# Kernel tuning notes

Measured on AMD Instinct MI355X. Metric: run time of the kernel, lower is better.

## Reference

```python
import jax, jax.numpy as jnp
import numpy as np

N_NODES = 100000
N_EDGES = 1600000
IN_DIM, HID_DIM, OUT_DIM = 128, 256, 512
BN_EPS = 1e-5


def setup_inputs() -> dict:
    key = jax.random.key(0)
    ks = jax.random.split(key, 10)
    x = jax.random.normal(ks[0], (N_NODES, IN_DIM), dtype=jnp.float32)
    edge_index = jax.random.randint(ks[1], (2, N_EDGES), 0, N_NODES, dtype=jnp.int64)
    def lin(k, o, i):
        return jax.random.normal(k, (o, i), dtype=jnp.float32) * (1.0 / np.sqrt(i))
    return {
        "x": x,
        "edge_index": edge_index,
        # SAGEConv 1: in_dim -> hidden_dim (lin_l has bias, lin_r has none)
        "W1l": lin(ks[2], HID_DIM, IN_DIM),
        "b1": jnp.zeros((HID_DIM,), dtype=jnp.float32),
        "W1r": lin(ks[3], HID_DIM, IN_DIM),
        # BatchNorm1d(hidden_dim)
        "gamma": jnp.ones((HID_DIM,), dtype=jnp.float32),
        "beta": jnp.zeros((HID_DIM,), dtype=jnp.float32),
        # SAGEConv 2: hidden_dim -> gnn_out_dim
        "W2l": lin(ks[4], OUT_DIM, HID_DIM),
        "b2": jnp.zeros((OUT_DIM,), dtype=jnp.float32),
        "W2r": lin(ks[5], OUT_DIM, HID_DIM),
    }


def _sage_max(h, src, dst, Wl, b, Wr, n_nodes):
    # gather source features, max-aggregate onto destination nodes
    agg = jax.ops.segment_max(h[src], dst, num_segments=n_nodes)  # [N, D]
    agg = jnp.where(jnp.isneginf(agg), 0.0, agg)  # PyG fills empty segments with 0
    return agg @ Wl.T + b + h @ Wr.T


def reference(x, edge_index, W1l, b1, W1r, gamma, beta, W2l, b2, W2r):
    src, dst = edge_index[0], edge_index[1]
    n = x.shape[0]
    # layer 1: SAGEConv(in_dim, hidden_dim, aggr='max')
    h = _sage_max(x, src, dst, W1l, b1, W1r, n)
    # BatchNorm1d (batch statistics), Dropout is identity in eval; no activation in 'sage' branch
    mean = jnp.mean(h, axis=0)
    var = jnp.var(h, axis=0)
    h = gamma * (h - mean) * jax.lax.rsqrt(var + BN_EPS) + beta
    # layer 2: SAGEConv(hidden_dim, gnn_out_dim, aggr='max')
    out = _sage_max(h, src, dst, W2l, b2, W2r, n)
    return out
```

## Files before the change

kernel.cpp:

```cpp
#include <hip/hip_runtime.h>
#include <hip/hip_bf16.h>
#include <stdint.h>

#define N_NODES 100000
#define N_EDGES 1600000
#define IN_DIM 128
#define HID_DIM 256
#define OUT_DIM 512
#define NBUK 391
#define BCAP 8192
#define EPB 4096

typedef __attribute__((ext_vector_type(4))) float f32x4;
typedef __attribute__((ext_vector_type(8))) short bf16x8;

__device__ __forceinline__ float bf16lo(uint32_t u){ uint32_t b = u << 16; return __builtin_bit_cast(float, b); }
__device__ __forceinline__ float bf16hi(uint32_t u){ uint32_t b = u & 0xffff0000u; return __builtin_bit_cast(float, b); }
__device__ __forceinline__ uint16_t f32_to_bf16(float f){
  uint32_t u = __builtin_bit_cast(uint32_t, f);
  uint32_t r = (u + 0x7fffu + ((u >> 16) & 1u)) >> 16;
  return (uint16_t)r;
}
__device__ __forceinline__ uint32_t pack_bf16_exact(float lo, float hi){
  return (__builtin_bit_cast(uint32_t, hi) & 0xffff0000u) | (__builtin_bit_cast(uint32_t, lo) >> 16);
}
__device__ __forceinline__ uint32_t pack_bf16_rne(float lo, float hi){
  return (uint32_t)f32_to_bf16(lo) | ((uint32_t)f32_to_bf16(hi) << 16);
}
__device__ __forceinline__ void gl2lds16(const void* g, void* l){
  __builtin_amdgcn_global_load_lds(
      (const __attribute__((address_space(1))) uint32_t*)g,
      (__attribute__((address_space(3))) uint32_t*)l, 16, 0, 0);
}

__global__ void k_convx(const float* __restrict__ x, uint16_t* __restrict__ X1x,
                        int* __restrict__ gcur, float* __restrict__ sum,
                        float* __restrict__ sumsq){
  if (blockIdx.x == 12500){
    const int t = threadIdx.x;
    for (int i = t; i < NBUK; i += 256) gcur[i] = i << 13;
    sum[t] = 0.f; sumsq[t] = 0.f;
    return;
  }
  const int idx = blockIdx.x * 256 + threadIdx.x;
  const int n = idx >> 5, q = idx & 31;
  const float4 v = *(const float4*)(x + (long)n * 128 + q * 4);
  ushort4 o;
  o.x = f32_to_bf16(v.x); o.y = f32_to_bf16(v.y);
  o.z = f32_to_bf16(v.z); o.w = f32_to_bf16(v.w);
  *(ushort4*)(X1x + (long)n * 128 + q * 4) = o;
}

__global__ void k_bucket(const int* __restrict__ src, const int* __restrict__ dst,
                         int* __restrict__ gcur, int* __restrict__ ebuk){
  __shared__ int hist[NBUK], curs[NBUK], base[NBUK];
  const int tid = threadIdx.x;
  const int e0 = blockIdx.x * EPB;
  for (int t = tid; t < NBUK; t += 256) hist[t] = 0;
  __syncthreads();
  for (int i = 0; i < EPB; i += 256){
    int e = e0 + i + tid;
    if (e < N_EDGES) atomicAdd(&hist[dst[e] >> 8], 1);
  }
  __syncthreads();
  for (int t = tid; t < NBUK; t += 256){
    int h = hist[t];
    base[t] = h ? atomicAdd(&gcur[t], h) : 0;
    curs[t] = 0;
  }
  __syncthreads();
  for (int i = 0; i < EPB; i += 256){
    int e = e0 + i + tid;
    if (e < N_EDGES){
      int d = dst[e];
      int b = d >> 8;
      int idx = atomicAdd(&curs[b], 1);
      int pos = base[b] + idx;
      if (pos < ((b + 1) << 13))
        ebuk[pos] = ((d & 255) << 17) | src[e];
    }
  }
}

__global__ __launch_bounds__(256)
void k_fillc(const int* __restrict__ gcur, const int* __restrict__ ebuk,
             int* __restrict__ row_start, int* __restrict__ esrc){
  __shared__ int ebuf[BCAP];
  __shared__ int cnt[256];
  __shared__ int wtot[4];
  __shared__ int red[4];
  const int b = blockIdx.x, tid = threadIdx.x, lane = tid & 63, wv = tid >> 6;
  const int nodebase = b << 8;
  const int nodecnt = min(256, N_NODES - nodebase);
  int accb = 0;
  for (int t = tid; t < b; t += 256) accb += gcur[t] - (t << 13);
  #pragma unroll
  for (int d = 32; d > 0; d >>= 1) accb += __shfl_xor(accb, d);
  if (lane == 0) red[wv] = accb;
  int size_b = gcur[b] - (b << 13);
  if (size_b > BCAP) size_b = BCAP;
  cnt[tid] = 0;
  for (int i = tid; i < size_b; i += 256) ebuf[i] = ebuk[(b << 13) + i];
  __syncthreads();
  const int bs = red[0] + red[1] + red[2] + red[3];
  for (int i = tid; i < size_b; i += 256) atomicAdd(&cnt[ebuf[i] >> 17], 1);
  __syncthreads();
  const int c = cnt[tid];
  int v = c;
  #pragma unroll
  for (int d = 1; d < 64; d <<= 1){ int t = __shfl_up(v, d); if (lane >= d) v += t; }
  if (lane == 63) wtot[wv] = v;
  __syncthreads();
  if (tid < 4){
    int t = wtot[tid];
    #pragma unroll
    for (int d = 1; d < 4; d <<= 1){ int u = __shfl_up(t, d); if (tid >= d) t += u; }
    wtot[tid] = t;
  }
  __syncthreads();
  const int excl = (wv ? wtot[wv - 1] : 0) + (v - c);
  if (tid < nodecnt) row_start[nodebase + tid] = bs + excl;
  if (b == NBUK - 1 && tid == 0) row_start[N_NODES] = N_EDGES;
  cnt[tid] = excl;
  __syncthreads();
  for (int i = tid; i < size_b; i += 256){
    int p = ebuf[i];
    int pos = atomicAdd(&cnt[p >> 17], 1);
    esrc[bs + pos] = p & 0x1FFFF;
  }
}

__global__ void k_w1(const float* __restrict__ W1l, const float* __restrict__ W1r,
                     uint16_t* __restrict__ W1cat){
  int idx = blockIdx.x * 256 + threadIdx.x;
  int j = idx >> 8, k = idx & 255;
  float v = (k < 128) ? W1l[j * 128 + k] : W1r[j * 128 + (k - 128)];
  W1cat[idx] = f32_to_bf16(v);
}

__global__ void k_w2(const float* __restrict__ W2l, const float* __restrict__ W2r,
                     const float* __restrict__ b2, const float* __restrict__ sum,
                     const float* __restrict__ sumsq, const float* __restrict__ gamma,
                     const float* __restrict__ beta, uint16_t* __restrict__ W2cat,
                     float* __restrict__ bias2, float* __restrict__ scale_g,
                     float* __restrict__ shift_g){
  __shared__ float sc_s[256], sh_s[256];
  const int tid = threadIdx.x;
  {
    const float inv_n = 1.0f / (float)N_NODES;
    float mean = sum[tid] * inv_n;
    float var = sumsq[tid] * inv_n - mean * mean;
    float sc = gamma[tid] * rsqrtf(var + 1e-5f);
    float sh = beta[tid] - mean * sc;
    sc_s[tid] = sc; sh_s[tid] = sh;
    if (blockIdx.x == 0){ scale_g[tid] = sc; shift_g[tid] = sh; }
  }
  __syncthreads();
  const int wid = (blockIdx.x * 256 + tid) >> 6;
  const int lane = tid & 63;
  float part = 0.f;
  #pragma unroll
  for (int t = 0; t < 4; t++){
    int k = t * 64 + lane;
    float wl = W2l[(long)wid * 256 + k];
    W2cat[(long)wid * 512 + k] = f32_to_bf16(wl);
    float wr = W2r[(long)wid * 256 + k];
    W2cat[(long)wid * 512 + 256 + k] = f32_to_bf16(wr * sc_s[k]);
    part += sh_s[k] * wr;
  }
  #pragma unroll
  for (int d = 32; d > 0; d >>= 1) part += __shfl_xor(part, d);
  if (lane == 0) bias2[wid] = b2[wid] + part;
}

__global__ void k_agg1(const uint32_t* __restrict__ X1x, const int* __restrict__ row_start,
                       const int* __restrict__ esrc, uint32_t* __restrict__ X1agg){
  const int wid = (blockIdx.x * 256 + threadIdx.x) >> 6;
  const int lane = threadIdx.x & 63;
  if (wid >= N_NODES) return;
  const int grp = lane >> 4, li = lane & 15;
  const int s0 = row_start[wid], s1 = row_start[wid + 1];
  float m[8];
  #pragma unroll
  for (int j = 0; j < 8; j++) m[j] = -INFINITY;

  #define ACC1(u)                                        \
    m[0] = fmaxf(m[0], bf16lo(u.x)); m[1] = fmaxf(m[1], bf16hi(u.x)); \
    m[2] = fmaxf(m[2], bf16lo(u.y)); m[3] = fmaxf(m[3], bf16hi(u.y)); \
    m[4] = fmaxf(m[4], bf16lo(u.z)); m[5] = fmaxf(m[5], bf16hi(u.z)); \
    m[6] = fmaxf(m[6], bf16lo(u.w)); m[7] = fmaxf(m[7], bf16hi(u.w));

  int e = s0 + grp;
  for (; e + 12 < s1; e += 16){
    const uint4 ua = *(const uint4*)(X1x + (long)esrc[e] * 64 + li * 4);
    const uint4 ub = *(const uint4*)(X1x + (long)esrc[e + 4] * 64 + li * 4);
    const uint4 uc = *(const uint4*)(X1x + (long)esrc[e + 8] * 64 + li * 4);
    const uint4 ud = *(const uint4*)(X1x + (long)esrc[e + 12] * 64 + li * 4);
    ACC1(ua); ACC1(ub); ACC1(uc); ACC1(ud);
  }
  for (; e < s1; e += 4){
    const uint4 u = *(const uint4*)(X1x + (long)esrc[e] * 64 + li * 4);
    ACC1(u);
  }
  #undef ACC1
  #pragma unroll
  for (int j = 0; j < 8; j++){
    m[j] = fmaxf(m[j], __shfl_xor(m[j], 16));
    m[j] = fmaxf(m[j], __shfl_xor(m[j], 32));
  }
  if (grp == 0){
    uint4 o;
    if (s1 == s0){ o.x = o.y = o.z = o.w = 0u; }
    else {
      o.x = pack_bf16_exact(m[0], m[1]);
      o.y = pack_bf16_exact(m[2], m[3]);
      o.z = pack_bf16_exact(m[4], m[5]);
      o.w = pack_bf16_exact(m[6], m[7]);
    }
    *(uint4*)(X1agg + (long)wid * 64 + li * 4) = o;
  }
}

__global__ void k_agg2(const uint32_t* __restrict__ X2h, const int* __restrict__ row_start,
                       const int* __restrict__ esrc, const float* __restrict__ scale,
                       const float* __restrict__ shift, uint32_t* __restrict__ X2agg){
  const int wid = (blockIdx.x * 256 + threadIdx.x) >> 6;
  const int lane = threadIdx.x & 63;
  if (wid >= N_NODES) return;
  const int half = lane >> 5, li = lane & 31;
  const int c0 = li * 8;
  const float4 sca = *(const float4*)(scale + c0);
  const float4 scb = *(const float4*)(scale + c0 + 4);
  const float4 sha = *(const float4*)(shift + c0);
  const float4 shb = *(const float4*)(shift + c0 + 4);
  const int s0 = row_start[wid], s1 = row_start[wid + 1];
  float m[8];
  #pragma unroll
  for (int j = 0; j < 8; j++) m[j] = -INFINITY;

  #define ACC8(u)                                                   \
    m[0] = fmaxf(m[0], fmaf(bf16lo(u.x), sca.x, sha.x));            \
    m[1] = fmaxf(m[1], fmaf(bf16hi(u.x), sca.y, sha.y));            \
    m[2] = fmaxf(m[2], fmaf(bf16lo(u.y), sca.z, sha.z));            \
    m[3] = fmaxf(m[3], fmaf(bf16hi(u.y), sca.w, sha.w));            \
    m[4] = fmaxf(m[4], fmaf(bf16lo(u.z), scb.x, shb.x));            \
    m[5] = fmaxf(m[5], fmaf(bf16hi(u.z), scb.y, shb.y));            \
    m[6] = fmaxf(m[6], fmaf(bf16lo(u.w), scb.z, shb.z));            \
    m[7] = fmaxf(m[7], fmaf(bf16hi(u.w), scb.w, shb.w));

  int e = s0 + half;
  for (; e + 6 < s1; e += 8){
    const uint4 ua = *(const uint4*)(X2h + (long)esrc[e] * 128 + li * 4);
    const uint4 ub = *(const uint4*)(X2h + (long)esrc[e + 2] * 128 + li * 4);
    const uint4 uc = *(const uint4*)(X2h + (long)esrc[e + 4] * 128 + li * 4);
    const uint4 ud = *(const uint4*)(X2h + (long)esrc[e + 6] * 128 + li * 4);
    ACC8(ua); ACC8(ub); ACC8(uc); ACC8(ud);
  }
  for (; e < s1; e += 2){
    const uint4 u = *(const uint4*)(X2h + (long)esrc[e] * 128 + li * 4);
    ACC8(u);
  }
  #undef ACC8
  #pragma unroll
  for (int j = 0; j < 8; j++) m[j] = fmaxf(m[j], __shfl_xor(m[j], 32));
  if (half == 0){
    uint4 o;
    if (s1 == s0){ o.x = 0u; o.y = 0u; o.z = 0u; o.w = 0u; }
    else {
      o.x = pack_bf16_rne(m[0], m[1]);
      o.y = pack_bf16_rne(m[2], m[3]);
      o.z = pack_bf16_rne(m[4], m[5]);
      o.w = pack_bf16_rne(m[6], m[7]);
    }
    *(uint4*)(X2agg + (long)wid * 128 + li * 4) = o;
  }
}

template<int KT, bool EPI1>
__global__ __launch_bounds__(256, 2)
void k_gemm(const uint16_t* __restrict__ Alo, const uint16_t* __restrict__ Ahi,
            const uint16_t* __restrict__ B, const float* __restrict__ bias,
            uint16_t* __restrict__ outb, float* __restrict__ outf,
            float* __restrict__ sum, float* __restrict__ sumsq)
{
  constexpr int NSTEPS = KT / 64;
  constexpr int HSTEPS = NSTEPS / 2;
  constexpr int NT = EPI1 ? 256 : 512;
  __shared__ uint8_t lds[2][32768];
  const int tid = threadIdx.x, lane = tid & 63, wv = tid >> 6;
  const int wvm = wv >> 1, wvn = wv & 1;
  const int nblk = blockIdx.x, mblk = blockIdx.y;

  f32x4 acc[4][4] = {};

  const int srow = wv * 32 + (lane >> 3);
  const int skb  = (lane & 7) * 16;

  const uint8_t* asrc_lo[4];
  const uint8_t* asrc_hi[4];
  const uint8_t* bsrc[4];
  #pragma unroll
  for (int i = 0; i < 4; i++){
    int row = srow + i * 8;
    int kbsw = skb ^ ((row & 7) << 4);
    long grow = (long)mblk * 128 + row;
    if (grow > N_NODES - 1) grow = N_NODES - 1;
    asrc_lo[i] = (const uint8_t*)Alo + grow * KT + kbsw;
    asrc_hi[i] = (const uint8_t*)Ahi + grow * KT + kbsw;
    bsrc[i] = (const uint8_t*)B + ((long)nblk * 128 + row) * (KT * 2) + kbsw;
  }

  #define STAGE(ks, buf)                                                     \
    _Pragma("unroll")                                                        \
    for (int i = 0; i < 4; i++)                                              \
      gl2lds16((ks) < HSTEPS ? asrc_lo[i] + (ks) * 128                       \
                             : asrc_hi[i] + ((ks) - HSTEPS) * 128,           \
               &lds[buf][(wv * 4 + i) * 1024]);                              \
    _Pragma("unroll")                                                        \
    for (int i = 0; i < 4; i++)                                              \
      gl2lds16(bsrc[i] + (ks) * 128, &lds[buf][16384 + (wv * 4 + i) * 1024]);

  STAGE(0, 0);

  #pragma unroll
  for (int ks = 0; ks < NSTEPS; ++ks){
    const int cur = ks & 1;
    if (ks + 1 < NSTEPS){
      STAGE(ks + 1, cur ^ 1);
      asm volatile("s_waitcnt vmcnt(8)" ::: "memory");
    } else {
      asm volatile("s_waitcnt vmcnt(0)" ::: "memory");
    }
    __builtin_amdgcn_s_barrier();
    asm volatile("" ::: "memory");

    const uint8_t* ldsA = &lds[cur][0];
    const uint8_t* ldsB = &lds[cur][16384];
    bf16x8 af[4][2], bfr[4][2];
    #pragma unroll
    for (int m = 0; m < 4; m++){
      int row = wvm * 64 + m * 16 + (lane & 15);
      #pragma unroll
      for (int kk = 0; kk < 2; kk++){
        int kb = kk * 64 + (lane >> 4) * 16;
        af[m][kk] = *(const bf16x8*)(ldsA + row * 128 + (kb ^ ((row & 7) << 4)));
      }
    }
    #pragma unroll
    for (int n = 0; n < 4; n++){
      int row = wvn * 64 + n * 16 + (lane & 15);
      #pragma unroll
      for (int kk = 0; kk < 2; kk++){
        int kb = kk * 64 + (lane >> 4) * 16;
        bfr[n][kk] = *(const bf16x8*)(ldsB + row * 128 + (kb ^ ((row & 7) << 4)));
      }
    }
    #pragma unroll
    for (int kk = 0; kk < 2; kk++)
      #pragma unroll
      for (int m = 0; m < 4; m++)
        #pragma unroll
        for (int n = 0; n < 4; n++)
          acc[m][n] = __builtin_amdgcn_mfma_f32_16x16x32_bf16(af[m][kk], bfr[n][kk], acc[m][n], 0, 0, 0);

    asm volatile("" ::: "memory");
    __builtin_amdgcn_s_barrier();
    asm volatile("" ::: "memory");
  }
  #undef STAGE

  const int rgrp = (lane >> 4) * 4;
  #pragma unroll
  for (int n = 0; n < 4; n++){
    const int col = nblk * 128 + wvn * 64 + n * 16 + (lane & 15);
    const float bv = bias[col];
    float s1v = 0.f, s2v = 0.f;
    #pragma unroll
    for (int m = 0; m < 4; m++){
      const int rowb = mblk * 128 + wvm * 64 + m * 16 + rgrp;
      f32x4 v = acc[m][n];
      #pragma unroll
      for (int j = 0; j < 4; j++){
        const int row = rowb + j;
        const float h = v[j] + bv;
        if (row < N_NODES){
          if (EPI1){
            outb[(long)row * NT + col] = f32_to_bf16(h);
            s1v += h; s2v += h * h;
          } else {
            __builtin_nontemporal_store(h, &outf[(long)row * NT + col]);
          }
        }
      }
    }
    if (EPI1){
      s1v += __shfl_xor(s1v, 16); s1v += __shfl_xor(s1v, 32);
      s2v += __shfl_xor(s2v, 16); s2v += __shfl_xor(s2v, 32);
      if (lane < 16){
        atomicAdd(&sum[col], s1v);
        atomicAdd(&sumsq[col], s2v);
      }
    }
  }
}

extern "C" void kernel_launch(void* const* d_in, const int* in_sizes, int n_in,
                              void* d_out, int out_size, void* d_ws, size_t ws_size,
                              hipStream_t stream){
  const float* x     = (const float*)d_in[0];
  const int*   ei    = (const int*)d_in[1];
  const float* W1l   = (const float*)d_in[2];
  const float* b1    = (const float*)d_in[3];
  const float* W1r   = (const float*)d_in[4];
  const float* gamma = (const float*)d_in[5];
  const float* beta  = (const float*)d_in[6];
  const float* W2l   = (const float*)d_in[7];
  const float* b2    = (const float*)d_in[8];
  const float* W2r   = (const float*)d_in[9];
  const int* esrc_in = ei;
  const int* edst_in = ei + N_EDGES;

  uint8_t* ws = (uint8_t*)d_ws;
  uint16_t* X1agg    = (uint16_t*)(ws + 0);
  uint16_t* X1x      = (uint16_t*)(ws + 25600000);
  uint16_t* X2agg    = (uint16_t*)(ws + 51200000);
  uint16_t* X2h      = (uint16_t*)(ws + 102400000);
  int* ebuk          = (int*)(ws + 51200000);
  int* esrc          = (int*)(ws + 153600000);
  int* row_start     = (int*)(ws + 160000000);
  int* gcur          = (int*)(ws + 160402176);
  uint16_t* W1cat    = (uint16_t*)(ws + 160800256);
  uint16_t* W2cat    = (uint16_t*)(ws + 160931328);
  float* bias2       = (float*)(ws + 161455616);
  float* sum         = (float*)(ws + 161457664);
  float* sumsq       = (float*)(ws + 161458688);
  float* scale       = (float*)(ws + 161459712);
  float* shift       = (float*)(ws + 161460736);

  hipLaunchKernelGGL(k_convx, dim3(12501), dim3(256), 0, stream, x, X1x, gcur, sum, sumsq);
  hipLaunchKernelGGL(k_bucket, dim3((N_EDGES + EPB - 1) / EPB), dim3(256), 0, stream,
                     esrc_in, edst_in, gcur, ebuk);
  hipLaunchKernelGGL(k_fillc, dim3(NBUK), dim3(256), 0, stream,
                     gcur, ebuk, row_start, esrc);

  hipLaunchKernelGGL(k_w1, dim3(256), dim3(256), 0, stream, W1l, W1r, W1cat);
  hipLaunchKernelGGL(k_agg1, dim3(25000), dim3(256), 0, stream,
                     (const uint32_t*)X1x, row_start, esrc, (uint32_t*)X1agg);

  hipLaunchKernelGGL((k_gemm<256, true>), dim3(2, 782), dim3(256), 0, stream,
                     X1agg, X1x, W1cat, b1, X2h, (float*)nullptr, sum, sumsq);

  hipLaunchKernelGGL(k_w2, dim3(128), dim3(256), 0, stream,
                     W2l, W2r, b2, sum, sumsq, gamma, beta, W2cat, bias2, scale, shift);

  hipLaunchKernelGGL(k_agg2, dim3(25000), dim3(256), 0, stream,
                     (const uint32_t*)X2h, row_start, esrc, scale, shift, (uint32_t*)X2agg);

  hipLaunchKernelGGL((k_gemm<512, false>), dim3(4, 782), dim3(256), 0, stream,
                     X2agg, X2h, W2cat, bias2, (uint16_t*)nullptr, (float*)d_out,
                     (float*)nullptr, (float*)nullptr);
}
```

Before: 412.9 us.

## Load GEMM fragments directly from global memory, dropping LDS staging

Removes the double-buffered LDS staging in the GEMM kernel, including the global_load_lds copies and barriers, and instead loads each MFMA operand fragment straight from global memory into registers. The launch bound's min-blocks hint is also dropped. The aim is to remove barrier and LDS traffic overhead and rely on L1/L2 caching for tile reuse across waves. In exchange, every wave re-fetches A and B rows from global memory, loads are narrower and less coalesced, and there is no software prefetch to hide latency.

```diff
diff --git a/kernel.cpp b/kernel.cpp
--- a/kernel.cpp
+++ b/kernel.cpp
@@ -26,11 +26,6 @@
 }
 __device__ __forceinline__ uint32_t pack_bf16_rne(float lo, float hi){
   return (uint32_t)f32_to_bf16(lo) | ((uint32_t)f32_to_bf16(hi) << 16);
-}
-__device__ __forceinline__ void gl2lds16(const void* g, void* l){
-  __builtin_amdgcn_global_load_lds(
-      (const __attribute__((address_space(1))) uint32_t*)g,
-      (__attribute__((address_space(3))) uint32_t*)l, 16, 0, 0);
 }
 
 __global__ void k_convx(const float* __restrict__ x, uint16_t* __restrict__ X1x,
@@ -277,7 +272,7 @@
 }
 
 template<int KT, bool EPI1>
-__global__ __launch_bounds__(256, 2)
+__global__ __launch_bounds__(256)
 void k_gemm(const uint16_t* __restrict__ Alo, const uint16_t* __restrict__ Ahi,
             const uint16_t* __restrict__ B, const float* __restrict__ bias,
             uint16_t* __restrict__ outb, float* __restrict__ outf,
@@ -286,88 +281,47 @@
   constexpr int NSTEPS = KT / 64;
   constexpr int HSTEPS = NSTEPS / 2;
   constexpr int NT = EPI1 ? 256 : 512;
-  __shared__ uint8_t lds[2][32768];
   const int tid = threadIdx.x, lane = tid & 63, wv = tid >> 6;
   const int wvm = wv >> 1, wvn = wv & 1;
   const int nblk = blockIdx.x, mblk = blockIdx.y;
 
   f32x4 acc[4][4] = {};
 
-  const int srow = wv * 32 + (lane >> 3);
-  const int skb  = (lane & 7) * 16;
-
-  const uint8_t* asrc_lo[4];
-  const uint8_t* asrc_hi[4];
-  const uint8_t* bsrc[4];
-  #pragma unroll
-  for (int i = 0; i < 4; i++){
-    int row = srow + i * 8;
-    int kbsw = skb ^ ((row & 7) << 4);
-    long grow = (long)mblk * 128 + row;
+  const int kbyte = (lane >> 4) * 16;
+
+  const uint8_t* aptr[4];
+  const uint8_t* bptr[4];
+  #pragma unroll
+  for (int m = 0; m < 4; m++){
+    long grow = (long)mblk * 128 + wvm * 64 + m * 16 + (lane & 15);
     if (grow > N_NODES - 1) grow = N_NODES - 1;
-    asrc_lo[i] = (const uint8_t*)Alo + grow * KT + kbsw;
-    asrc_hi[i] = (const uint8_t*)Ahi + grow * KT + kbsw;
-    bsrc[i] = (const uint8_t*)B + ((long)nblk * 128 + row) * (KT * 2) + kbsw;
-  }
-
-  #define STAGE(ks, buf)                                                     \
-    _Pragma("unroll")                                                        \
-    for (int i = 0; i < 4; i++)                                              \
-      gl2lds16((ks) < HSTEPS ? asrc_lo[i] + (ks) * 128                       \
-                             : asrc_hi[i] + ((ks) - HSTEPS) * 128,           \
-               &lds[buf][(wv * 4 + i) * 1024]);                              \
-    _Pragma("unroll")                                                        \
-    for (int i = 0; i < 4; i++)                                              \
-      gl2lds16(bsrc[i] + (ks) * 128, &lds[buf][16384 + (wv * 4 + i) * 1024]);
-
-  STAGE(0, 0);
+    aptr[m] = (const uint8_t*)Alo + grow * KT + kbyte;
+  }
+  #pragma unroll
+  for (int n = 0; n < 4; n++){
+    long brow = (long)nblk * 128 + wvn * 64 + n * 16 + (lane & 15);
+    bptr[n] = (const uint8_t*)B + brow * (KT * 2) + kbyte;
+  }
+  const long ahi_off = (const uint8_t*)Ahi - (const uint8_t*)Alo;
 
   #pragma unroll
   for (int ks = 0; ks < NSTEPS; ++ks){
-    const int cur = ks & 1;
-    if (ks + 1 < NSTEPS){
-      STAGE(ks + 1, cur ^ 1);
-      asm volatile("s_waitcnt vmcnt(8)" ::: "memory");
-    } else {
-      asm volatile("s_waitcnt vmcnt(0)" ::: "memory");
-    }
-    __builtin_amdgcn_s_barrier();
-    asm volatile("" ::: "memory");
-
-    const uint8_t* ldsA = &lds[cur][0];
-    const uint8_t* ldsB = &lds[cur][16384];
-    bf16x8 af[4][2], bfr[4][2];
+    const long aoff = (ks < HSTEPS) ? (long)ks * 128 : ahi_off + (long)(ks - HSTEPS) * 128;
+    const long boff = (long)ks * 128;
     #pragma unroll
-    for (int m = 0; m < 4; m++){
-      int row = wvm * 64 + m * 16 + (lane & 15);
+    for (int kk = 0; kk < 2; kk++){
+      bf16x8 af[4], bfr[4];
       #pragma unroll
-      for (int kk = 0; kk < 2; kk++){
-        int kb = kk * 64 + (lane >> 4) * 16;
-        af[m][kk] = *(const bf16x8*)(ldsA + row * 128 + (kb ^ ((row & 7) << 4)));
-      }
-    }
-    #pragma unroll
-    for (int n = 0; n < 4; n++){
-      int row = wvn * 64 + n * 16 + (lane & 15);
+      for (int m = 0; m < 4; m++) af[m] = *(const bf16x8*)(aptr[m] + aoff + kk * 64);
       #pragma unroll
-      for (int kk = 0; kk < 2; kk++){
-        int kb = kk * 64 + (lane >> 4) * 16;
-        bfr[n][kk] = *(const bf16x8*)(ldsB + row * 128 + (kb ^ ((row & 7) << 4)));
-      }
-    }
-    #pragma unroll
-    for (int kk = 0; kk < 2; kk++)
+      for (int n = 0; n < 4; n++) bfr[n] = *(const bf16x8*)(bptr[n] + boff + kk * 64);
       #pragma unroll
       for (int m = 0; m < 4; m++)
         #pragma unroll
         for (int n = 0; n < 4; n++)
-          acc[m][n] = __builtin_amdgcn_mfma_f32_16x16x32_bf16(af[m][kk], bfr[n][kk], acc[m][n], 0, 0, 0);
-
-    asm volatile("" ::: "memory");
-    __builtin_amdgcn_s_barrier();
-    asm volatile("" ::: "memory");
-  }
-  #undef STAGE
+          acc[m][n] = __builtin_amdgcn_mfma_f32_16x16x32_bf16(af[m], bfr[n], acc[m][n], 0, 0, 0);
+    }
+  }
 
   const int rgrp = (lane >> 4) * 4;
   #pragma unroll
```

New measurement: 549.0 us. 33.0% more time.
